# Performance work log

Measured on AMD Instinct MI355X. Metric: run time of the kernel, lower is better.

## Reference

```python
import jax, jax.numpy as jnp
import numpy as np

IN_C = 256
OUT_C = 256
KS = 3
PAD = 1
EPS = 1e-5
BLOCK_SIZE = 256  # largest power of 2 dividing IN_C
NUM_BLOCKS = IN_C // BLOCK_SIZE


def golay_sequence(n):
    pow2 = 1
    while pow2 < n:
        pow2 *= 2
    a = np.array([1.0], dtype=np.float32)
    b = np.array([1.0], dtype=np.float32)
    while len(a) < pow2:
        a, b = np.concatenate([a, b]), np.concatenate([a, -b])
    return a[:n]


def fwht(x):
    """Unnormalized fast Walsh-Hadamard transform over the last axis (Sylvester order)."""
    base = x.shape[:-1]
    n = x.shape[-1]
    h = 1
    while h < n:
        y = x.reshape(base + (n // (2 * h), 2, h))
        a, c = y[..., 0, :], y[..., 1, :]
        x = jnp.stack([a + c, a - c], axis=-2).reshape(base + (n,))
        h *= 2
    return x


def setup_inputs() -> dict:
    key = jax.random.key(0)
    k1, k2, k3 = jax.random.split(key, 3)
    x = jax.random.normal(k1, (32, IN_C, 56, 56), dtype=jnp.float32)
    fan_in = IN_C * KS * KS
    W = jax.random.normal(k2, (OUT_C, IN_C, KS, KS), dtype=jnp.float32) / np.sqrt(fan_in)
    b = jax.random.normal(k3, (OUT_C,), dtype=jnp.float32) * 0.01
    rms_w = jnp.ones((IN_C,), dtype=jnp.float32)
    return {"x": x, "W": W, "b": b, "rms_w": rms_w}


def reference(x, W, b, rms_w):
    n, c, h, w = x.shape
    golay = jnp.asarray(golay_sequence(c)).reshape(1, c, 1, 1)
    x = x * golay                                    # Golay elementwise multiply
    x = jnp.transpose(x, (0, 2, 3, 1))               # NCHW -> NHWC
    x = x.reshape(n, h, w, NUM_BLOCKS, BLOCK_SIZE)
    x = fwht(x)                                      # blockwise Hadamard butterfly
    x = x.reshape(n, h, w, c)
    # RMSNorm over channel dim
    x = x * jax.lax.rsqrt(jnp.mean(x * x, axis=-1, keepdims=True) + EPS) * rms_w
    x = jnp.transpose(x, (0, 3, 1, 2))               # NHWC -> NCHW
    out = jax.lax.conv_general_dilated(
        x, W, window_strides=(1, 1), padding=((PAD, PAD), (PAD, PAD)),
        dimension_numbers=("NCHW", "OIHW", "NCHW"))
    return out + b[None, :, None, None]
```

## Files before the change

kernel.cpp:

```cpp
#include <hip/hip_runtime.h>
#include <hip/hip_bf16.h>

typedef short v8s __attribute__((ext_vector_type(8)));
typedef float v4f __attribute__((ext_vector_type(4)));
typedef float v16f __attribute__((ext_vector_type(16)));
typedef unsigned short u16;

#define PROW 58
#define PCOL 64

static constexpr size_t A_CC_STRIDE = (size_t)32 * PROW * PCOL * 32;
static constexpr size_t A_BYTES     = 8 * A_CC_STRIDE * 2;
static constexpr size_t WB_ELEMS    = (size_t)9 * 8 * 256 * 32;

__device__ __forceinline__ void gl2lds16(const void* gptr, void* lptr) {
  auto g = (const __attribute__((address_space(1))) unsigned int*)gptr;
  auto l = (__attribute__((address_space(3))) unsigned int*)lptr;
  __builtin_amdgcn_global_load_lds(g, l, 16, 0, 0);
}

__device__ __forceinline__ u16 f2bf(float f) {
  __hip_bfloat16 h = __float2bfloat16(f);
  union { __hip_bfloat16 b; u16 u; } cv; cv.b = h; return cv.u;
}

__global__ __launch_bounds__(256, 2) void fwht_kernel(
    const float* __restrict__ x, const float* __restrict__ rms_w,
    u16* __restrict__ A)
{
  __shared__ __align__(16) char smem[58368];
  float* tile = (float*)smem;
  u16*   ob   = (u16*)smem;

  const int tid = threadIdx.x;
  const int y = blockIdx.x;
  const int n = blockIdx.y;
  const float* src = x + (size_t)n * 256 * 3136 + (size_t)y * 56;
  for (int f = tid; f < 256 * 56; f += 256) {
    int ch = f / 56;
    int xx = f - ch * 56;
    tile[ch * 57 + xx] = src[(size_t)ch * 3136 + xx];
  }
  __syncthreads();

  const int lane = tid & 63;
  const int wv = tid >> 6;
  float gs[4], rw[4];
  #pragma unroll
  for (int k = 0; k < 4; k++) {
    int ch = lane + 64 * k;
    gs[k] = 1.0f - 2.0f * (float)(__popc(ch & (ch >> 1)) & 1);
    rw[k] = rms_w[ch];
  }

  unsigned int res[14][2];
  #pragma unroll
  for (int i = 0; i < 14; i++) {
    const int p = wv + 4 * i;
    float v[4];
    #pragma unroll
    for (int k = 0; k < 4; k++)
      v[k] = tile[(lane + 64 * k) * 57 + p] * gs[k];
    #pragma unroll
    for (int hs = 0; hs < 6; hs++) {
      const int h = 1 << hs;
      #pragma unroll
      for (int k = 0; k < 4; k++) {
        float o = __shfl_xor(v[k], h, 64);
        v[k] = ((lane & h) ? -v[k] : v[k]) + o;
      }
    }
    { float a=v[0], b=v[1], c=v[2], d=v[3];
      v[0]=a+b; v[1]=a-b; v[2]=c+d; v[3]=c-d; }
    { float a=v[0], b=v[1], c=v[2], d=v[3];
      v[0]=a+c; v[2]=a-c; v[1]=b+d; v[3]=b-d; }
    float ss = v[0]*v[0] + v[1]*v[1] + v[2]*v[2] + v[3]*v[3];
    #pragma unroll
    for (int hs = 0; hs < 6; hs++) ss += __shfl_xor(ss, 1 << hs, 64);
    float sc = rsqrtf(ss * (1.0f / 256.0f) + 1e-5f);
    res[i][0] = (unsigned int)f2bf(v[0] * sc * rw[0]) |
                ((unsigned int)f2bf(v[1] * sc * rw[1]) << 16);
    res[i][1] = (unsigned int)f2bf(v[2] * sc * rw[2]) |
                ((unsigned int)f2bf(v[3] * sc * rw[3]) << 16);
  }
  __syncthreads();

  const int icq = (lane >> 3) & 3;
  const int jj = lane & 7;
  const int ccl = lane >> 5;
  #pragma unroll
  for (int i = 0; i < 14; i++) {
    const int p = wv + 4 * i;
    const int sw = ((p + 1) >> 1) & 3;
    const int qs = (icq ^ sw) * 8 + jj;
    #pragma unroll
    for (int k = 0; k < 4; k++) {
      const int cc = 2 * k + ccl;
      u16 val = (u16)(res[i][k >> 1] >> (16 * (k & 1)));
      ob[cc * 1808 + p * 32 + qs] = val;
    }
  }
  __syncthreads();

  const int row = y + 1;
  #pragma unroll
  for (int i = 0; i < 7; i++) {
    int c = tid + 256 * i;
    int cc = c / 224, rem = c - cc * 224;
    v8s val = *(const v8s*)(ob + cc * 1808 + rem * 8);
    size_t go = (((size_t)cc * 32 + n) * PROW + row) * 2048 + 32 + rem * 8;
    *(v8s*)(A + go) = val;
  }
  {
    const v8s z = {0,0,0,0,0,0,0,0};
    int cc = tid >> 5, s = tid & 31;
    size_t rb = (((size_t)cc * 32 + n) * PROW + row) * 2048;
    if (s < 4) *(v8s*)(A + rb + s * 8) = z;
    else       *(v8s*)(A + rb + 57 * 32 + (s - 4) * 8) = z;
  }
  if (y == 0 || y == 55) {
    const v8s z = {0,0,0,0,0,0,0,0};
    const int r = (y == 0) ? 0 : 57;
    #pragma unroll
    for (int i = 0; i < 8; i++) {
      int c = tid + 256 * i;
      int cc = c >> 8, rem = c & 255;
      size_t go = (((size_t)cc * 32 + n) * PROW + r) * 2048 + rem * 8;
      *(v8s*)(A + go) = z;
    }
  }
}

__global__ __launch_bounds__(256) void wconv_kernel(
    const float* __restrict__ Wf, u16* __restrict__ Wb)
{
  int t = blockIdx.x * 256 + threadIdx.x;
  int j = t & 7;
  int icq_st = (t >> 3) & 3;
  int oc = (t >> 5) & 255;
  int cc = (t >> 13) & 7;
  int kk = t >> 16;
  int icq = icq_st ^ ((oc >> 1) & 3);
  int ic = cc * 32 + icq * 8 + j;
  int ky = kk / 3, kx = kk - ky * 3;
  float w = Wf[((oc * 256 + ic) * 3 + ky) * 3 + kx];
  Wb[t] = f2bf(w);
}

__global__ __launch_bounds__(256, 3) void conv_kernel(
    const u16* __restrict__ A, const u16* __restrict__ Wb,
    const float* __restrict__ bias, float* __restrict__ out)
{
  __shared__ __align__(16) u16 As[4 * PCOL * 32];
  __shared__ __align__(16) u16 Bs[3 * 128 * 32];

  const int tid  = threadIdx.x;
  const int lane = tid & 63;
  const int wv   = tid >> 6;
  const int wm   = wv & 1;
  const int wn   = wv >> 1;
  const int m31  = lane & 31;
  const int kh8  = lane >> 5;

  const int ocb = blockIdx.x;
  const int y0  = blockIdx.y * 2;
  const int n   = blockIdx.z;

  const u16* gA = A + ((size_t)n * PROW + y0) * 2048;

  v16f acc[2][2];
  #pragma unroll
  for (int i = 0; i < 2; i++)
    #pragma unroll
    for (int j = 0; j < 2; j++)
      #pragma unroll
      for (int e = 0; e < 16; e++)
        acc[i][j][e] = 0.0f;

  int ub[2][2];
  #pragma unroll
  for (int nf = 0; nf < 2; nf++)
    #pragma unroll
    for (int kh = 0; kh < 2; kh++) {
      int ocl = wn * 64 + nf * 32 + m31;
      int q = kh * 2 + kh8;
      ub[nf][kh] = (ocl * 4 + (q ^ ((ocl >> 1) & 3))) * 8;
    }

  auto stageA = [&](int cc) {
    const u16* g = gA + (size_t)cc * A_CC_STRIDE + tid * 8;
    u16* d = As + tid * 8;
    #pragma unroll
    for (int k = 0; k < 4; k++)
      gl2lds16(g + k * 2048, d + k * 2048);
  };
  auto stageB = [&](int cc, int ky) {
    #pragma unroll
    for (int kx = 0; kx < 3; kx++) {
      const int kk = ky * 3 + kx;
      const u16* g = Wb + ((kk * 8 + cc) * 8192 + ocb * 4096) + tid * 8;
      u16* d = Bs + kx * 4096 + tid * 8;
      gl2lds16(g, d);
      gl2lds16(g + 2048, d + 2048);
    }
  };

  for (int cc = 0; cc < 8; cc++) {
    __syncthreads();
    stageA(cc);
    stageB(cc, 0);
    __syncthreads();
    #pragma unroll
    for (int ky = 0; ky < 3; ky++) {
      #pragma unroll
      for (int kx = 0; kx < 3; kx++) {
        v8s af[2][2];
        #pragma unroll
        for (int mf = 0; mf < 2; mf++)
          #pragma unroll
          for (int kh = 0; kh < 2; kh++) {
            int col = mf * 32 + m31 + kx;
            col = col > 63 ? 63 : col;
            int q = kh * 2 + kh8;
            int ua = (((wm + ky) * PCOL + col) * 4 + (q ^ ((col >> 1) & 3))) * 8;
            af[mf][kh] = *(const v8s*)(As + ua);
          }
        v8s bf[2][2];
        const u16* bsb = Bs + kx * 4096;
        #pragma unroll
        for (int nf = 0; nf < 2; nf++)
          #pragma unroll
          for (int kh = 0; kh < 2; kh++)
            bf[nf][kh] = *(const v8s*)(bsb + ub[nf][kh]);
        #pragma unroll
        for (int mf = 0; mf < 2; mf++)
          #pragma unroll
          for (int nf = 0; nf < 2; nf++) {
            acc[mf][nf] = __builtin_amdgcn_mfma_f32_32x32x16_bf16(af[mf][0], bf[nf][0], acc[mf][nf], 0, 0, 0);
            acc[mf][nf] = __builtin_amdgcn_mfma_f32_32x32x16_bf16(af[mf][1], bf[nf][1], acc[mf][nf], 0, 0, 0);
          }
      }
      if (ky < 2) {
        __syncthreads();
        stageB(cc, ky + 1);
        __syncthreads();
      }
    }
  }

  const int yrow = y0 + wm;
  #pragma unroll
  for (int nf = 0; nf < 2; nf++) {
    const int oc = ocb * 128 + wn * 64 + nf * 32 + m31;
    const float bb = bias[oc];
    float* orow = out + ((size_t)(n * 256 + oc) * 56 + yrow) * 56;
    #pragma unroll
    for (int mf = 0; mf < 2; mf++) {
      #pragma unroll
      for (int g = 0; g < 4; g++) {
        const int x0 = mf * 32 + 8 * g + 4 * kh8;
        if (x0 < 56) {
          v4f val = { acc[mf][nf][4*g+0] + bb, acc[mf][nf][4*g+1] + bb,
                      acc[mf][nf][4*g+2] + bb, acc[mf][nf][4*g+3] + bb };
          *(v4f*)(orow + x0) = val;
        }
      }
    }
  }
}

extern "C" void kernel_launch(void* const* d_in, const int* in_sizes, int n_in,
                              void* d_out, int out_size, void* d_ws, size_t ws_size,
                              hipStream_t stream)
{
  const float* x     = (const float*)d_in[0];
  const float* Wf    = (const float*)d_in[1];
  const float* bias  = (const float*)d_in[2];
  const float* rms_w = (const float*)d_in[3];
  float* out = (float*)d_out;

  if (ws_size < A_BYTES + WB_ELEMS * 2) return;

  u16* Abf = (u16*)d_ws;
  u16* Wb  = (u16*)((char*)d_ws + A_BYTES);

  fwht_kernel<<<dim3(56, 32), 256, 0, stream>>>(x, rms_w, Abf);
  wconv_kernel<<<dim3((int)(WB_ELEMS / 256)), 256, 0, stream>>>(Wf, Wb);
  conv_kernel<<<dim3(2, 28, 32), 256, 0, stream>>>(Abf, Wb, bias, out);
}
```

Before: 342.3 us.

## Load weights directly into registers and double-buffer input tiles in LDS

Weights are no longer staged through shared memory. Each lane loads its B fragments from global memory straight into registers, through a three-deep register ring that prefetches two kernel taps ahead. The input tile is double-buffered in LDS so the next channel chunk loads while the current one is being computed, which cuts the number of barriers per chunk from six to one. The weight layout drops its XOR swizzle to suit the direct register loads. In exchange, register pressure rises and weight traffic goes through the global/L2 path without reuse across waves in LDS.

```diff
diff --git a/kernel.cpp b/kernel.cpp
--- a/kernel.cpp
+++ b/kernel.cpp
@@ -135,15 +135,12 @@
     const float* __restrict__ Wf, u16* __restrict__ Wb)
 {
   int t = blockIdx.x * 256 + threadIdx.x;
-  int j = t & 7;
-  int icq_st = (t >> 3) & 3;
+  int ic = t & 31;
   int oc = (t >> 5) & 255;
   int cc = (t >> 13) & 7;
   int kk = t >> 16;
-  int icq = icq_st ^ ((oc >> 1) & 3);
-  int ic = cc * 32 + icq * 8 + j;
   int ky = kk / 3, kx = kk - ky * 3;
-  float w = Wf[((oc * 256 + ic) * 3 + ky) * 3 + kx];
+  float w = Wf[((oc * 256 + cc * 32 + ic) * 3 + ky) * 3 + kx];
   Wb[t] = f2bf(w);
 }
 
@@ -151,8 +148,7 @@
     const u16* __restrict__ A, const u16* __restrict__ Wb,
     const float* __restrict__ bias, float* __restrict__ out)
 {
-  __shared__ __align__(16) u16 As[4 * PCOL * 32];
-  __shared__ __align__(16) u16 Bs[3 * 128 * 32];
+  __shared__ __align__(16) u16 As[2][4 * PCOL * 32];
 
   const int tid  = threadIdx.x;
   const int lane = tid & 63;
@@ -167,6 +163,7 @@
   const int n   = blockIdx.z;
 
   const u16* gA = A + ((size_t)n * PROW + y0) * 2048;
+  const u16* Bp = Wb + (ocb * 128 + wn * 64 + m31) * 32 + kh8 * 8;
 
   v16f acc[2][2];
   #pragma unroll
@@ -177,75 +174,61 @@
       for (int e = 0; e < 16; e++)
         acc[i][j][e] = 0.0f;
 
-  int ub[2][2];
-  #pragma unroll
-  for (int nf = 0; nf < 2; nf++)
-    #pragma unroll
-    for (int kh = 0; kh < 2; kh++) {
-      int ocl = wn * 64 + nf * 32 + m31;
-      int q = kh * 2 + kh8;
-      ub[nf][kh] = (ocl * 4 + (q ^ ((ocl >> 1) & 3))) * 8;
-    }
-
-  auto stageA = [&](int cc) {
+  auto stageA = [&](int cc, int buf) {
     const u16* g = gA + (size_t)cc * A_CC_STRIDE + tid * 8;
-    u16* d = As + tid * 8;
+    u16* d = As[buf] + tid * 8;
     #pragma unroll
     for (int k = 0; k < 4; k++)
       gl2lds16(g + k * 2048, d + k * 2048);
   };
-  auto stageB = [&](int cc, int ky) {
-    #pragma unroll
-    for (int kx = 0; kx < 3; kx++) {
-      const int kk = ky * 3 + kx;
-      const u16* g = Wb + ((kk * 8 + cc) * 8192 + ocb * 4096) + tid * 8;
-      u16* d = Bs + kx * 4096 + tid * 8;
-      gl2lds16(g, d);
-      gl2lds16(g + 2048, d + 2048);
-    }
+  auto loadB = [&](v8s* dst, int cc, int kk) {
+    const u16* p = Bp + (size_t)(kk * 8 + cc) * 8192;
+    #pragma unroll
+    for (int nf = 0; nf < 2; nf++)
+      #pragma unroll
+      for (int kh = 0; kh < 2; kh++)
+        dst[nf * 2 + kh] = *(const v8s*)(p + nf * 1024 + kh * 16);
   };
 
+  v8s Br[3][4];
+  loadB(Br[0], 0, 0);
+  loadB(Br[1], 0, 1);
+  stageA(0, 0);
+  __syncthreads();
+
   for (int cc = 0; cc < 8; cc++) {
+    if (cc < 7) stageA(cc + 1, (cc + 1) & 1);
+    const u16* asb = As[cc & 1];
+    #pragma unroll
+    for (int kk = 0; kk < 9; kk++) {
+      {
+        int pcc = cc, pkk = kk + 2;
+        if (pkk > 8) { pkk -= 9; pcc = cc + 1; }
+        if (pcc < 8) loadB(Br[(kk + 2) % 3], pcc, pkk);
+      }
+      const int ky = kk / 3;
+      const int kx = kk - ky * 3;
+      v8s af[2][2];
+      #pragma unroll
+      for (int mf = 0; mf < 2; mf++)
+        #pragma unroll
+        for (int kh = 0; kh < 2; kh++) {
+          int col = mf * 32 + m31 + kx;
+          col = col > 63 ? 63 : col;
+          int q = kh * 2 + kh8;
+          int ua = (((wm + ky) * PCOL + col) * 4 + (q ^ ((col >> 1) & 3))) * 8;
+          af[mf][kh] = *(const v8s*)(asb + ua);
+        }
+      const v8s* b = Br[kk % 3];
+      #pragma unroll
+      for (int mf = 0; mf < 2; mf++)
+        #pragma unroll
+        for (int nf = 0; nf < 2; nf++) {
+          acc[mf][nf] = __builtin_amdgcn_mfma_f32_32x32x16_bf16(af[mf][0], b[nf * 2 + 0], acc[mf][nf], 0, 0, 0);
+          acc[mf][nf] = __builtin_amdgcn_mfma_f32_32x32x16_bf16(af[mf][1], b[nf * 2 + 1], acc[mf][nf], 0, 0, 0);
+        }
+    }
     __syncthreads();
-    stageA(cc);
-    stageB(cc, 0);
-    __syncthreads();
-    #pragma unroll
-    for (int ky = 0; ky < 3; ky++) {
-      #pragma unroll
-      for (int kx = 0; kx < 3; kx++) {
-        v8s af[2][2];
-        #pragma unroll
-        for (int mf = 0; mf < 2; mf++)
-          #pragma unroll
-          for (int kh = 0; kh < 2; kh++) {
-            int col = mf * 32 + m31 + kx;
-            col = col > 63 ? 63 : col;
-            int q = kh * 2 + kh8;
-            int ua = (((wm + ky) * PCOL + col) * 4 + (q ^ ((col >> 1) & 3))) * 8;
-            af[mf][kh] = *(const v8s*)(As + ua);
-          }
-        v8s bf[2][2];
-        const u16* bsb = Bs + kx * 4096;
-        #pragma unroll
-        for (int nf = 0; nf < 2; nf++)
-          #pragma unroll
-          for (int kh = 0; kh < 2; kh++)
-            bf[nf][kh] = *(const v8s*)(bsb + ub[nf][kh]);
-        #pragma unroll
-        for (int mf = 0; mf < 2; mf++)
-          #pragma unroll
-          for (int nf = 0; nf < 2; nf++) {
-            acc[mf][nf] = __builtin_amdgcn_mfma_f32_32x32x16_bf16(af[mf][0], bf[nf][0], acc[mf][nf], 0, 0, 0);
-            acc[mf][nf] = __builtin_amdgcn_mfma_f32_32x32x16_bf16(af[mf][1], bf[nf][1], acc[mf][nf], 0, 0, 0);
-          }
-      }
-      if (ky < 2) {
-        __syncthreads();
-        stageB(cc, ky + 1);
-        __syncthreads();
-      }
-    }
   }
 
   const int yrow = y0 + wm;
```

Result: slower. 360.9 us (+5.4%).
